# Optimization experiments

Measured on AMD Instinct MI355X. Metric: run time of the kernel, lower is better.

Reference implementation:

```python
import jax, jax.numpy as jnp
import numpy as np

TAU = 1.5      # lif_tau
V_TH = 1.0     # spikingjelly default v_threshold
EPS = 1e-5     # BatchNorm eps
ALPHA = 4.0    # spikingjelly default sigmoid surrogate alpha

@jax.custom_vjp
def spike_fn(x):
    return (x >= 0.0).astype(x.dtype)

def _spike_fwd(x):
    return spike_fn(x), x

def _spike_bwd(x, g):
    s = jax.nn.sigmoid(ALPHA * x)
    return (g * ALPHA * s * (1.0 - s),)

spike_fn.defvjp(_spike_fwd, _spike_bwd)

def lif(x):
    # x: [T, B, C, N]; hard reset to 0, decay_input=True, detach_reset=True
    def step(v, xt):
        v = v + (xt - v) / TAU
        s = spike_fn(v - V_TH)
        sd = jax.lax.stop_gradient(s)
        v = (1.0 - sd) * v
        return v, s
    _, spikes = jax.lax.scan(step, jnp.zeros_like(x[0]), x)
    return spikes

def bn(x, gamma, beta, mean, var):
    # eval-mode BatchNorm1d over channel dim of [B, C, L]
    inv = gamma * jax.lax.rsqrt(var + EPS)
    return x * inv[None, :, None] + (beta - mean * inv)[None, :, None]

def setup_inputs() -> dict:
    key = jax.random.key(0)
    ks = jax.random.split(key, 13)
    B, C, T, N, H = 8, 256, 4, 4096, 1024
    return {
        "x": jax.random.normal(ks[0], (B, C, T, N), jnp.float32),
        "fc1_w": jax.random.normal(ks[1], (H, C), jnp.float32) * 0.05,
        "fc1_b": jax.random.normal(ks[2], (H,), jnp.float32) * 0.05,
        "fc2_w": jax.random.normal(ks[3], (C, H), jnp.float32) * 0.05,
        "fc2_b": jax.random.normal(ks[4], (C,), jnp.float32) * 0.05,
        "bn1_gamma": jax.random.uniform(ks[5], (H,), jnp.float32, 0.5, 1.5),
        "bn1_beta": jax.random.normal(ks[6], (H,), jnp.float32) * 0.1,
        "bn1_mean": jax.random.normal(ks[7], (H,), jnp.float32) * 0.1,
        "bn1_var": jax.random.uniform(ks[8], (H,), jnp.float32, 0.5, 1.5),
        "bn2_gamma": jax.random.uniform(ks[9], (C,), jnp.float32, 0.5, 1.5),
        "bn2_beta": jax.random.normal(ks[10], (C,), jnp.float32) * 0.1,
        "bn2_mean": jax.random.normal(ks[11], (C,), jnp.float32) * 0.1,
        "bn2_var": jax.random.uniform(ks[12], (C,), jnp.float32, 0.5, 1.5),
    }

def reference(x, fc1_w, fc1_b, fc2_w, fc2_b,
              bn1_gamma, bn1_beta, bn1_mean, bn1_var,
              bn2_gamma, bn2_beta, bn2_mean, bn2_var):
    B, C, T, N = x.shape
    H = fc1_w.shape[0]
    # fc2_bn on raw input, then LIF over T
    h = bn(x.reshape(B, C, T * N), bn2_gamma, bn2_beta, bn2_mean, bn2_var)
    h = h.reshape(B, C, T, N).transpose(2, 0, 1, 3)          # [T,B,C,N]
    h = lif(h).transpose(1, 2, 0, 3).reshape(B, C, T * N)    # [B,C,TN]
    # fc1: 1x1 conv == GEMM over channels
    h = jnp.einsum('hc,bcl->bhl', fc1_w, h) + fc1_b[None, :, None]
    h = bn(h, bn1_gamma, bn1_beta, bn1_mean, bn1_var)
    h = h.reshape(B, H, T, N).transpose(2, 0, 1, 3)          # [T,B,H,N]
    h = lif(h).transpose(1, 2, 0, 3).reshape(B, H, T * N)    # [B,H,TN]
    # fc2
    h = jnp.einsum('ch,bhl->bcl', fc2_w, h) + fc2_b[None, :, None]
    return h.reshape(B, C, T, N)
```

## Files before the change

### kernel.cpp

```cpp
#include <hip/hip_runtime.h>

#define BB 8
#define CC 256
#define TT 4
#define NNv 4096
#define HH 1024
#define LLv (TT*NNv)

typedef short bf16x8 __attribute__((ext_vector_type(8)));
typedef float f32x4 __attribute__((ext_vector_type(4)));

static __device__ __forceinline__ float bfbits2f(unsigned short h) {
    return __uint_as_float(((unsigned int)h) << 16);
}
static __device__ __forceinline__ unsigned short f2bf(float f) {
    unsigned int u = __float_as_uint(f);
    return (unsigned short)((u + 0x7FFFu + ((u >> 16) & 1u)) >> 16);
}
static __device__ __forceinline__ int permpos(int j) { return (j >> 1) + ((j & 1) << 2); }

static __device__ __forceinline__ uint4 spikes8_to_bf16(unsigned long long d) {
    unsigned int lo = (unsigned int)d, hi = (unsigned int)(d >> 32);
    uint4 o;
    o.x = (lo & 0x10001u) * 0x3F80u;
    o.y = (hi & 0x10001u) * 0x3F80u;
    o.z = ((lo >> 8) & 0x10001u) * 0x3F80u;
    o.w = ((hi >> 8) & 0x10001u) * 0x3F80u;
    return o;
}

static __device__ __forceinline__ void barrier_keep_vmem() {
    asm volatile("s_waitcnt lgkmcnt(0)" ::: "memory");
    __builtin_amdgcn_s_barrier();
    __builtin_amdgcn_sched_barrier(0);
}

__global__ __launch_bounds__(256) void k_prep1(const float* __restrict__ w,
                                               unsigned short* __restrict__ wf)
{
    int i = blockIdx.x * 256 + threadIdx.x;
    int h = i >> 8, c = i & 255;
    int ht = h >> 6, hr = h & 63, g = hr >> 4, ln = hr & 15;
    int ko = c >> 6, cr = c & 63, kb = cr >> 5, q = (cr >> 3) & 3, j = c & 7;
    size_t base = (((((size_t)ht * 4 + ko) * 2 + kb) * 4 + g) * 64 + q * 16 + ln) * 8 + permpos(j);
    const size_t WS = 262144;
    float x = w[i];
    unsigned short hi = f2bf(x); float r  = __fsub_rn(x, bfbits2f(hi));
    unsigned short md = f2bf(r); float r2 = __fsub_rn(r, bfbits2f(md));
    unsigned short lo = f2bf(r2);
    wf[base] = hi; wf[WS + base] = md; wf[2 * WS + base] = lo;
}

__global__ __launch_bounds__(256) void k_prep2(const float* __restrict__ w,
                                               unsigned short* __restrict__ wf)
{
    int i = blockIdx.x * 256 + threadIdx.x;
    int c = i >> 10, h = i & 1023;
    int ct = c >> 6, cr = c & 63, g = cr >> 4, ln = cr & 15;
    int ko = h >> 7, hr = h & 127, kb = hr >> 5, q = (hr >> 3) & 3, j = h & 7;
    size_t base = (((((size_t)ct * 8 + ko) * 4 + kb) * 4 + g) * 64 + q * 16 + ln) * 8 + permpos(j);
    const size_t WS = 262144;
    float x = w[i];
    unsigned short hi = f2bf(x); float r = __fsub_rn(x, bfbits2f(hi));
    unsigned short lo = f2bf(r);
    wf[base] = hi; wf[WS + base] = lo;
}

__global__ __launch_bounds__(256) void k_bn2_lif_t(
    const float* __restrict__ x,
    const float* __restrict__ g, const float* __restrict__ be,
    const float* __restrict__ mu, const float* __restrict__ va,
    unsigned char* __restrict__ s1T, int b0)
{
    __shared__ unsigned char ts[TT][64][80];
    int tx = threadIdx.x;
    int n0 = blockIdx.x * 64;
    int c0 = blockIdx.y * 64;
    int bl = blockIdx.z;
    int b  = b0 + bl;
    int cl = tx >> 2, np = tx & 3;
    int c = c0 + cl;
    float rsq = __fdiv_rn(1.0f, __fsqrt_rn(__fadd_rn(va[c], 1e-5f)));
    float inv = __fmul_rn(g[c], rsq);
    float add = __fsub_rn(be[c], __fmul_rn(mu[c], inv));
    size_t xb = ((size_t)(b * CC + c) * TT) * NNv + n0 + np * 16;
    float v[16];
    #pragma unroll
    for (int i = 0; i < 16; i++) v[i] = 0.0f;
    #pragma unroll
    for (int t = 0; t < TT; t++) {
        float4 p[4];
        #pragma unroll
        for (int k = 0; k < 4; k++) p[k] = *(const float4*)(x + xb + (size_t)t * NNv + 4 * k);
        const float* xp = (const float*)p;
        unsigned int ob[4] = {0, 0, 0, 0};
        #pragma unroll
        for (int i = 0; i < 16; i++) {
            float y = __fadd_rn(__fmul_rn(xp[i], inv), add);
            float vv = __fadd_rn(v[i], __fdiv_rn(__fsub_rn(y, v[i]), 1.5f));
            bool sp = vv >= 1.0f;
            v[i] = sp ? 0.0f : vv;
            if (sp) ob[i >> 2] |= 1u << (8 * (i & 3));
        }
        uint4 pk; pk.x = ob[0]; pk.y = ob[1]; pk.z = ob[2]; pk.w = ob[3];
        *(uint4*)&ts[t][cl][np * 16] = pk;
    }
    __syncthreads();
    int nl = tx >> 2, cp = tx & 3;
    #pragma unroll
    for (int t = 0; t < TT; t++) {
        unsigned int u[4];
        #pragma unroll
        for (int kk = 0; kk < 4; kk++) {
            u[kk] = (unsigned int)ts[t][cp * 16 + kk * 4 + 0][nl]
                  | ((unsigned int)ts[t][cp * 16 + kk * 4 + 1][nl] << 8)
                  | ((unsigned int)ts[t][cp * 16 + kk * 4 + 2][nl] << 16)
                  | ((unsigned int)ts[t][cp * 16 + kk * 4 + 3][nl] << 24);
        }
        uint4 pk; pk.x = u[0]; pk.y = u[1]; pk.z = u[2]; pk.w = u[3];
        *(uint4*)(s1T + ((size_t)(bl * TT + t) * NNv + n0 + nl) * CC + c0 + cp * 16) = pk;
    }
}

__global__ __launch_bounds__(256) void k_gemm1_lif(
    const unsigned short* __restrict__ w1f,
    const float* __restrict__ b1,
    const float* __restrict__ g1, const float* __restrict__ be1,
    const float* __restrict__ mu1, const float* __restrict__ va1,
    const unsigned char* __restrict__ s1T, unsigned char* __restrict__ s2T)
{
    __shared__ unsigned short Ss[2][TT][64][72];
    const int tx = threadIdx.x;
    const int n0 = blockIdx.x * 64;
    const int ht = blockIdx.y;
    const int bl = blockIdx.z;
    const int lane = tx & 63, w = tx >> 6;
    const int q = lane >> 4, ln = lane & 15;
    const int mh = (w & 1) * 32, wn = (w >> 1) * 32;
    const int h0 = ht * 64;
    const size_t WS = 262144;

    f32x4 acc[TT][2][2];
    #pragma unroll
    for (int t = 0; t < TT; t++)
    #pragma unroll
    for (int mi = 0; mi < 2; mi++)
    #pragma unroll
    for (int ni = 0; ni < 2; ni++)
        acc[t][mi][ni] = (f32x4){0.f, 0.f, 0.f, 0.f};

    unsigned long long d[8];
    #pragma unroll
    for (int i = 0; i < 8; i++) {
        int task = i * 256 + tx;
        int cb = task & 7, nr = (task >> 3) & 63, t = task >> 9;
        d[i] = *(const unsigned long long*)(
            s1T + ((size_t)(bl * TT + t) * NNv + n0 + nr) * CC + 0 * 64 + cb * 8);
    }

    for (int ko = 0; ko < 4; ko++) {
        const int cur = ko & 1;
        #pragma unroll
        for (int i = 0; i < 8; i++) {
            int task = i * 256 + tx;
            int cb = task & 7, nr = (task >> 3) & 63, t = task >> 9;
            *(uint4*)&Ss[cur][t][nr][cb * 8] = spikes8_to_bf16(d[i]);
        }
        if (ko < 3) {
            #pragma unroll
            for (int i = 0; i < 8; i++) {
                int task = i * 256 + tx;
                int cb = task & 7, nr = (task >> 3) & 63, t = task >> 9;
                d[i] = *(const unsigned long long*)(
                    s1T + ((size_t)(bl * TT + t) * NNv + n0 + nr) * CC + (ko + 1) * 64 + cb * 8);
            }
        }
        barrier_keep_vmem();

        #pragma unroll
        for (int kb = 0; kb < 2; kb++) {
            bf16x8 wf[2][3];
            #pragma unroll
            for (int mi = 0; mi < 2; mi++) {
                int gg = (mh >> 4) + mi;
                size_t fbase = (((((size_t)ht * 4 + ko) * 2 + kb) * 4 + gg) * 64 + lane) * 8;
                #pragma unroll
                for (int s = 0; s < 3; s++)
                    wf[mi][s] = *(const bf16x8*)(w1f + s * WS + fbase);
            }
            #pragma unroll
            for (int t = 0; t < TT; t++) {
                bf16x8 sf0 = *(const bf16x8*)&Ss[cur][t][wn + ln][kb * 32 + q * 8];
                bf16x8 sf1 = *(const bf16x8*)&Ss[cur][t][wn + 16 + ln][kb * 32 + q * 8];
                #pragma unroll
                for (int s = 0; s < 3; s++) {
                    acc[t][0][0] = __builtin_amdgcn_mfma_f32_16x16x32_bf16(wf[0][s], sf0, acc[t][0][0], 0, 0, 0);
                    acc[t][0][1] = __builtin_amdgcn_mfma_f32_16x16x32_bf16(wf[0][s], sf1, acc[t][0][1], 0, 0, 0);
                    acc[t][1][0] = __builtin_amdgcn_mfma_f32_16x16x32_bf16(wf[1][s], sf0, acc[t][1][0], 0, 0, 0);
                    acc[t][1][1] = __builtin_amdgcn_mfma_f32_16x16x32_bf16(wf[1][s], sf1, acc[t][1][1], 0, 0, 0);
                }
            }
        }
    }

    #pragma unroll
    for (int mi = 0; mi < 2; mi++) {
        float invr[4], addr_[4], biasr[4];
        #pragma unroll
        for (int r = 0; r < 4; r++) {
            int h = h0 + mh + mi * 16 + q * 4 + r;
            float rsq = __fdiv_rn(1.0f, __fsqrt_rn(__fadd_rn(va1[h], 1e-5f)));
            invr[r] = __fmul_rn(g1[h], rsq);
            addr_[r] = __fsub_rn(be1[h], __fmul_rn(mu1[h], invr[r]));
            biasr[r] = b1[h];
        }
        #pragma unroll
        for (int ni = 0; ni < 2; ni++) {
            int l_n = n0 + wn + ni * 16 + ln;
            float v4[4] = {0.f, 0.f, 0.f, 0.f};
            #pragma unroll
            for (int t = 0; t < TT; t++) {
                unsigned int pk = 0;
                #pragma unroll
                for (int r = 0; r < 4; r++) {
                    float h1 = __fadd_rn(acc[t][mi][ni][r], biasr[r]);
                    float y  = __fadd_rn(__fmul_rn(h1, invr[r]), addr_[r]);
                    float vv = __fadd_rn(v4[r], __fdiv_rn(__fsub_rn(y, v4[r]), 1.5f));
                    bool sp = vv >= 1.0f;
                    v4[r] = sp ? 0.0f : vv;
                    if (sp) pk |= (1u << (8 * r));
                }
                *(unsigned int*)(s2T + ((size_t)bl * LLv + t * NNv + l_n) * HH
                                 + h0 + mh + mi * 16 + q * 4) = pk;
            }
        }
    }
}

__global__ __launch_bounds__(256) void k_gemm2(
    const unsigned short* __restrict__ w2f,
    const float* __restrict__ b2c,
    const unsigned char* __restrict__ s2T, float* __restrict__ outp, int b0)
{
    __shared__ unsigned short Ss[2][128][136];
    const int tx = threadIdx.x;
    const int l0 = blockIdx.x * 128;
    const int ct = blockIdx.y;
    const int bl = blockIdx.z;
    const int b  = b0 + bl;
    const int lane = tx & 63, w = tx >> 6;
    const int q = lane >> 4, ln = lane & 15;
    const int mc = (w & 1) * 32, wl = (w >> 1) * 64;
    const size_t WS = 262144;

    f32x4 acc[2][4];
    #pragma unroll
    for (int mi = 0; mi < 2; mi++)
    #pragma unroll
    for (int ni = 0; ni < 4; ni++)
        acc[mi][ni] = (f32x4){0.f, 0.f, 0.f, 0.f};

    unsigned long long d[8];
    #pragma unroll
    for (int i = 0; i < 8; i++) {
        int task = i * 256 + tx;
        int hb = task & 15, lr = task >> 4;
        d[i] = *(const unsigned long long*)(
            s2T + ((size_t)bl * LLv + l0 + lr) * HH + 0 * 128 + hb * 8);
    }

    for (int ko = 0; ko < 8; ko++) {
        const int cur = ko & 1;
        #pragma unroll
        for (int i = 0; i < 8; i++) {
            int task = i * 256 + tx;
            int hb = task & 15, lr = task >> 4;
            *(uint4*)&Ss[cur][lr][hb * 8] = spikes8_to_bf16(d[i]);
        }
        if (ko < 7) {
            #pragma unroll
            for (int i = 0; i < 8; i++) {
                int task = i * 256 + tx;
                int hb = task & 15, lr = task >> 4;
                d[i] = *(const unsigned long long*)(
                    s2T + ((size_t)bl * LLv + l0 + lr) * HH + (ko + 1) * 128 + hb * 8);
            }
        }
        barrier_keep_vmem();

        #pragma unroll
        for (int kb = 0; kb < 4; kb++) {
            bf16x8 wf[2][2];
            #pragma unroll
            for (int mi = 0; mi < 2; mi++) {
                int gg = (mc >> 4) + mi;
                size_t fbase = (((((size_t)ct * 8 + ko) * 4 + kb) * 4 + gg) * 64 + lane) * 8;
                #pragma unroll
                for (int s = 0; s < 2; s++)
                    wf[mi][s] = *(const bf16x8*)(w2f + s * WS + fbase);
            }
            bf16x8 sf[4];
            #pragma unroll
            for (int ni = 0; ni < 4; ni++)
                sf[ni] = *(const bf16x8*)&Ss[cur][wl + ni * 16 + ln][kb * 32 + q * 8];
            #pragma unroll
            for (int s = 0; s < 2; s++)
            #pragma unroll
            for (int mi = 0; mi < 2; mi++)
            #pragma unroll
            for (int ni = 0; ni < 4; ni++)
                acc[mi][ni] = __builtin_amdgcn_mfma_f32_16x16x32_bf16(wf[mi][s], sf[ni], acc[mi][ni], 0, 0, 0);
        }
    }
    #pragma unroll
    for (int mi = 0; mi < 2; mi++)
    #pragma unroll
    for (int r = 0; r < 4; r++) {
        int c = ct * 64 + mc + mi * 16 + q * 4 + r;
        float bias = b2c[c];
        #pragma unroll
        for (int ni = 0; ni < 4; ni++) {
            int l = l0 + wl + ni * 16 + ln;
            outp[((size_t)b * CC + c) * LLv + l] = __fadd_rn(acc[mi][ni][r], bias);
        }
    }
}

extern "C" void kernel_launch(void* const* d_in, const int* in_sizes, int n_in,
                              void* d_out, int out_size, void* d_ws, size_t ws_size,
                              hipStream_t stream) {
    const float* x    = (const float*)d_in[0];
    const float* fc1w = (const float*)d_in[1];
    const float* fc1b = (const float*)d_in[2];
    const float* fc2w = (const float*)d_in[3];
    const float* fc2b = (const float*)d_in[4];
    const float* g1   = (const float*)d_in[5];
    const float* be1  = (const float*)d_in[6];
    const float* mu1  = (const float*)d_in[7];
    const float* va1  = (const float*)d_in[8];
    const float* g2   = (const float*)d_in[9];
    const float* be2  = (const float*)d_in[10];
    const float* mu2  = (const float*)d_in[11];
    const float* va2  = (const float*)d_in[12];

    const size_t WB  = (size_t)(3 + 2) * 262144 * sizeof(unsigned short);
    const size_t S1B = (size_t)TT * NNv * CC;
    const size_t S2B = (size_t)LLv * HH;

    int nbc;
    bool full_s1;
    if      (ws_size >= WB + 8 * S1B + 8 * S2B) { nbc = 8; full_s1 = true;  }
    else if (ws_size >= WB + 8 * S1B + 4 * S2B) { nbc = 4; full_s1 = true;  }
    else if (ws_size >= WB + 8 * S1B + 2 * S2B) { nbc = 2; full_s1 = true;  }
    else if (ws_size >= WB + 8 * S1B + 1 * S2B) { nbc = 1; full_s1 = true;  }
    else                                        { nbc = 1; full_s1 = false; }

    unsigned short* w1f = (unsigned short*)d_ws;
    unsigned short* w2f = w1f + (size_t)3 * 262144;
    unsigned char*  s1T = (unsigned char*)(w2f + (size_t)2 * 262144);
    unsigned char*  s2T = s1T + (full_s1 ? (size_t)8 * S1B : S1B);
    float* outp = (float*)d_out;

    hipLaunchKernelGGL(k_prep1, dim3(1024), dim3(256), 0, stream, fc1w, w1f);
    hipLaunchKernelGGL(k_prep2, dim3(1024), dim3(256), 0, stream, fc2w, w2f);

    if (full_s1) {
        hipLaunchKernelGGL(k_bn2_lif_t, dim3(NNv / 64, CC / 64, BB), dim3(256), 0, stream,
                           x, g2, be2, mu2, va2, s1T, 0);
        for (int b0 = 0; b0 < BB; b0 += nbc) {
            hipLaunchKernelGGL(k_gemm1_lif, dim3(NNv / 64, HH / 64, nbc), dim3(256), 0, stream,
                               w1f, fc1b, g1, be1, mu1, va1, s1T + (size_t)b0 * S1B, s2T);
            hipLaunchKernelGGL(k_gemm2, dim3(LLv / 128, CC / 64, nbc), dim3(256), 0, stream,
                               w2f, fc2b, s2T, outp, b0);
        }
    } else {
        for (int b0 = 0; b0 < BB; ++b0) {
            hipLaunchKernelGGL(k_bn2_lif_t, dim3(NNv / 64, CC / 64, 1), dim3(256), 0, stream,
                               x, g2, be2, mu2, va2, s1T, b0);
            hipLaunchKernelGGL(k_gemm1_lif, dim3(NNv / 64, HH / 64, 1), dim3(256), 0, stream,
                               w1f, fc1b, g1, be1, mu1, va1, s1T, s2T);
            hipLaunchKernelGGL(k_gemm2, dim3(LLv / 128, CC / 64, 1), dim3(256), 0, stream,
                               w2f, fc2b, s2T, outp, b0);
        }
    }
}
```

Before: 658.5 us.

## Single-buffer LDS tiles and double-buffer prefetch registers in both GEMM kernels

Both GEMM kernels drop the double-buffered LDS tile in favour of a single one. To keep loads overlapping, the global-prefetch register array becomes double-buffered and an extra barrier is placed before each LDS overwrite. The K loop is fully unrolled so the register-buffer indices resolve at compile time, and __launch_bounds__(256,3) asks for three blocks per CU. The aim is more resident blocks per CU through lower LDS use, paid for with an extra barrier per K-step and tighter register limits that could cause spills.

```diff
diff --git a/kernel.cpp b/kernel.cpp
--- a/kernel.cpp
+++ b/kernel.cpp
@@ -122,14 +122,14 @@
     }
 }
 
-__global__ __launch_bounds__(256) void k_gemm1_lif(
+__global__ __launch_bounds__(256, 3) void k_gemm1_lif(
     const unsigned short* __restrict__ w1f,
     const float* __restrict__ b1,
     const float* __restrict__ g1, const float* __restrict__ be1,
     const float* __restrict__ mu1, const float* __restrict__ va1,
     const unsigned char* __restrict__ s1T, unsigned char* __restrict__ s2T)
 {
-    __shared__ unsigned short Ss[2][TT][64][72];
+    __shared__ unsigned short Ss[TT][64][72];
     const int tx = threadIdx.x;
     const int n0 = blockIdx.x * 64;
     const int ht = blockIdx.y;
@@ -149,29 +149,31 @@
     for (int ni = 0; ni < 2; ni++)
         acc[t][mi][ni] = (f32x4){0.f, 0.f, 0.f, 0.f};
 
-    unsigned long long d[8];
+    unsigned long long d[2][8];
     #pragma unroll
     for (int i = 0; i < 8; i++) {
         int task = i * 256 + tx;
         int cb = task & 7, nr = (task >> 3) & 63, t = task >> 9;
-        d[i] = *(const unsigned long long*)(
+        d[0][i] = *(const unsigned long long*)(
             s1T + ((size_t)(bl * TT + t) * NNv + n0 + nr) * CC + 0 * 64 + cb * 8);
     }
 
+    #pragma unroll
     for (int ko = 0; ko < 4; ko++) {
         const int cur = ko & 1;
+        if (ko > 0) barrier_keep_vmem();
         #pragma unroll
         for (int i = 0; i < 8; i++) {
             int task = i * 256 + tx;
             int cb = task & 7, nr = (task >> 3) & 63, t = task >> 9;
-            *(uint4*)&Ss[cur][t][nr][cb * 8] = spikes8_to_bf16(d[i]);
+            *(uint4*)&Ss[t][nr][cb * 8] = spikes8_to_bf16(d[cur][i]);
         }
         if (ko < 3) {
             #pragma unroll
             for (int i = 0; i < 8; i++) {
                 int task = i * 256 + tx;
                 int cb = task & 7, nr = (task >> 3) & 63, t = task >> 9;
-                d[i] = *(const unsigned long long*)(
+                d[cur ^ 1][i] = *(const unsigned long long*)(
                     s1T + ((size_t)(bl * TT + t) * NNv + n0 + nr) * CC + (ko + 1) * 64 + cb * 8);
             }
         }
@@ -190,8 +192,8 @@
             }
             #pragma unroll
             for (int t = 0; t < TT; t++) {
-                bf16x8 sf0 = *(const bf16x8*)&Ss[cur][t][wn + ln][kb * 32 + q * 8];
-                bf16x8 sf1 = *(const bf16x8*)&Ss[cur][t][wn + 16 + ln][kb * 32 + q * 8];
+                bf16x8 sf0 = *(const bf16x8*)&Ss[t][wn + ln][kb * 32 + q * 8];
+                bf16x8 sf1 = *(const bf16x8*)&Ss[t][wn + 16 + ln][kb * 32 + q * 8];
                 #pragma unroll
                 for (int s = 0; s < 3; s++) {
                     acc[t][0][0] = __builtin_amdgcn_mfma_f32_16x16x32_bf16(wf[0][s], sf0, acc[t][0][0], 0, 0, 0);
@@ -237,12 +239,12 @@
     }
 }
 
-__global__ __launch_bounds__(256) void k_gemm2(
+__global__ __launch_bounds__(256, 3) void k_gemm2(
     const unsigned short* __restrict__ w2f,
     const float* __restrict__ b2c,
     const unsigned char* __restrict__ s2T, float* __restrict__ outp, int b0)
 {
-    __shared__ unsigned short Ss[2][128][136];
+    __shared__ unsigned short Ss[128][136];
     const int tx = threadIdx.x;
     const int l0 = blockIdx.x * 128;
     const int ct = blockIdx.y;
@@ -260,29 +262,31 @@
     for (int ni = 0; ni < 4; ni++)
         acc[mi][ni] = (f32x4){0.f, 0.f, 0.f, 0.f};
 
-    unsigned long long d[8];
+    unsigned long long d[2][8];
     #pragma unroll
     for (int i = 0; i < 8; i++) {
         int task = i * 256 + tx;
         int hb = task & 15, lr = task >> 4;
-        d[i] = *(const unsigned long long*)(
+        d[0][i] = *(const unsigned long long*)(
             s2T + ((size_t)bl * LLv + l0 + lr) * HH + 0 * 128 + hb * 8);
     }
 
+    #pragma unroll
     for (int ko = 0; ko < 8; ko++) {
         const int cur = ko & 1;
+        if (ko > 0) barrier_keep_vmem();
         #pragma unroll
         for (int i = 0; i < 8; i++) {
             int task = i * 256 + tx;
             int hb = task & 15, lr = task >> 4;
-            *(uint4*)&Ss[cur][lr][hb * 8] = spikes8_to_bf16(d[i]);
+            *(uint4*)&Ss[lr][hb * 8] = spikes8_to_bf16(d[cur][i]);
         }
         if (ko < 7) {
             #pragma unroll
             for (int i = 0; i < 8; i++) {
                 int task = i * 256 + tx;
                 int hb = task & 15, lr = task >> 4;
-                d[i] = *(const unsigned long long*)(
+                d[cur ^ 1][i] = *(const unsigned long long*)(
                     s2T + ((size_t)bl * LLv + l0 + lr) * HH + (ko + 1) * 128 + hb * 8);
             }
         }
@@ -302,7 +306,7 @@
             bf16x8 sf[4];
             #pragma unroll
             for (int ni = 0; ni < 4; ni++)
-                sf[ni] = *(const bf16x8*)&Ss[cur][wl + ni * 16 + ln][kb * 32 + q * 8];
+                sf[ni] = *(const bf16x8*)&Ss[wl + ni * 16 + ln][kb * 32 + q * 8];
             #pragma unroll
             for (int s = 0; s < 2; s++)
             #pragma unroll
```

After: 597.2 us. 9.3% less time.
